# Kernel optimization log

Hardware: AMD Instinct MI355X
Metric: run time of the kernel (lower is better)

## Reference

```python
import jax, jax.numpy as jnp
import numpy as np

STATE_DIM = 64   # state_dim (N), N/2 complex modes
KLEN = 128       # L, learned impulse-response length
CH = 1           # channel_dim
BATCH = 32
T = 1048576      # sequence length (T > L -> FFT branch)
DT_MIN, DT_MAX = 0.001, 0.1


def setup_inputs() -> dict:
    key = jax.random.key(0)
    ks = jax.random.split(key, 7)
    N2 = STATE_DIM // 2
    x = jax.random.normal(ks[0], (BATCH, CH, T), dtype=jnp.float32)
    # HiPPO initialization: w = -0.5 + i * (1/pi) * N * (N/(1+2k) - 1)
    k = np.arange(N2)
    w_real = np.broadcast_to(np.float32(-0.5), (CH, N2)).copy()
    w_imag = np.broadcast_to(
        ((1.0 / np.pi) * STATE_DIM * (STATE_DIM / (1.0 + 2.0 * k) - 1.0)).astype(np.float32),
        (CH, N2)).copy()
    log_dt = (jax.random.uniform(ks[1], (CH, 1), dtype=jnp.float32)
              * (np.log(DT_MAX) - np.log(DT_MIN)) + np.log(DT_MIN))
    C_real = jax.random.normal(ks[2], (CH, 1, N2), dtype=jnp.float32) * 0.1
    C_imag = jax.random.normal(ks[3], (CH, 1, N2), dtype=jnp.float32) * 0.1
    B_real = jax.random.normal(ks[4], (CH, N2), dtype=jnp.float32)
    B_imag = jax.random.normal(ks[5], (CH, N2), dtype=jnp.float32)
    nrm = jnp.sqrt(jnp.sum(B_real ** 2 + B_imag ** 2, axis=-1, keepdims=True))
    B_real, B_imag = B_real / nrm, B_imag / nrm
    D = jax.random.normal(ks[6], (CH,), dtype=jnp.float32) * 0.1
    return {"azimuth_data": x,
            "w_real": jnp.asarray(w_real), "w_imag": jnp.asarray(w_imag),
            "log_dt": log_dt,
            "C_real": C_real, "C_imag": C_imag,
            "B_real": B_real, "B_imag": B_imag,
            "D": D}


def _ssm_kernel(w_real, w_imag, log_dt, C_real, C_imag, B_real, B_imag, D, L):
    """Vectorized equivalent of the per-step power recurrence: h_k = Re(sum_n C_n B_n A_n^k)."""
    w = w_real + 1j * w_imag                      # (CH, N2) complex eigenvalues
    dt = jnp.exp(log_dt)                          # (CH, 1)
    Cc = C_real + 1j * C_imag                     # (CH, 1, N2)
    Bc = B_real + 1j * B_imag                     # (CH, N2)
    dtA = dt[..., None] * w                       # (CH,1,1)*(CH,N2) -> (CH,1,N2)
    # coefficients C.squeeze(1) * B, with the same broadcast as torch: (CH,N2)*(CH,1,N2)->(CH,1,N2)
    coef = jnp.squeeze(Cc, axis=1) * (jnp.ones_like(dtA) * Bc)   # (CH,1,N2)
    ks = jnp.arange(L, dtype=dtA.real.dtype)                      # (L,)
    Ak = jnp.exp(dtA[..., None] * ks)                             # (CH,1,N2,L) = A_discrete**k
    h = jnp.real(jnp.sum(coef[..., None] * Ak, axis=-2))          # (CH,1,L)
    h = h.at[..., 0].add(D)                                       # hk[0] += D (broadcast (CH,1)+(CH,))
    return h[:, None]                                             # unsqueeze(1) -> (CH,1,1,L)


def reference(azimuth_data, w_real, w_imag, log_dt, C_real, C_imag, B_real, B_imag, D):
    Bsz, Cn, Tn = azimuth_data.shape
    kernel = _ssm_kernel(w_real, w_imag, log_dt, C_real, C_imag, B_real, B_imag, D, KLEN)
    pad = KLEN - 1
    x_padded = jnp.pad(azimuth_data, ((0, 0), (0, 0), (pad, 0)))   # causal left-pad
    L_conv = x_padded.shape[-1]
    x_f = jnp.fft.rfft(x_padded, n=L_conv)                         # (B, CH, F)
    k_f = jnp.fft.rfft(kernel, n=L_conv)                           # (CH, 1, 1, F)
    y_f = x_f * k_f                                                # broadcast -> (CH, B, 1, F)
    focused = jnp.fft.irfft(y_f, n=L_conv)[..., :Tn]               # (CH, B, 1, T) — matches torch broadcast
    return focused
```

## Files before the change

kernel.cpp:

```cpp
#include <hip/hip_runtime.h>

#define T_LEN  1048576
#define NROWS  32
#define NTAPS  128
#define N2     32
#define BLOCK  256
#define SEG    4096
#define SEGS_PER_ROW 256
#define HALO   256
#define NCH    11
#define STG_F32 (SEG + HALO)
#define STG_Q4  (STG_F32 / 4)
#define XH_BYTES 8704
#define SMEM_BYTES (XH_BYTES + 4 * 1024 * 4)

typedef __attribute__((ext_vector_type(8)))  _Float16 half8;
typedef __attribute__((ext_vector_type(2)))  __fp16   fp16x2;
typedef __attribute__((ext_vector_type(16))) float    f32x16;
typedef __attribute__((ext_vector_type(4)))  float    f32x4;

__device__ __forceinline__ int swz16(int q) { return q ^ ((q >> 3) & 7); }

__global__ __launch_bounds__(NTAPS) void ssm_taps(
    const float* __restrict__ w_real, const float* __restrict__ w_imag,
    const float* __restrict__ log_dt,
    const float* __restrict__ C_real, const float* __restrict__ C_imag,
    const float* __restrict__ B_real, const float* __restrict__ B_imag,
    const float* __restrict__ Dp, float* __restrict__ ws) {
  __shared__ float hsh[NTAPS];
  const int k = threadIdx.x;
  const float dt = expf(log_dt[0]);
  const float kf = (float)k;
  float acc = 0.f;
  for (int n = 0; n < N2; ++n) {
    const float a  = dt * w_real[n];
    const float b  = dt * w_imag[n];
    const float cr = C_real[n], ci = C_imag[n];
    const float br = B_real[n], bi = B_imag[n];
    const float coef_r = cr * br - ci * bi;
    const float coef_i = cr * bi + ci * br;
    const float e = expf(a * kf);
    float s, c;
    sincosf(b * kf, &s, &c);
    acc += e * (coef_r * c - coef_i * s);
  }
  if (k == 0) acc += Dp[0];
  ws[k]  = acc;
  hsh[k] = acc;
  __syncthreads();
  if (k < 64) {
    _Float16* AH = (_Float16*)(ws + NTAPS);
    const int m = k & 31, g = k >> 5;
    for (int c = 0; c < NCH; ++c)
      for (int i = 0; i < 8; ++i) {
        const int idx = m + 129 - 16 * c - 8 * g - i;
        const float v = (idx >= 0 && idx < NTAPS) ? hsh[idx] : 0.f;
        AH[(c * 64 + k) * 8 + i] = (_Float16)v;
      }
  }
}

__global__ __launch_bounds__(BLOCK, 6) void ssm_conv(
    const float* __restrict__ x, const float* __restrict__ ws,
    float* __restrict__ out) {
  __shared__ __align__(16) unsigned char smem[SMEM_BYTES];
  _Float16* xh    = (_Float16*)smem;
  float*    ebase = (float*)(smem + XH_BYTES);

  const int tid  = threadIdx.x;
  const int lane = tid & 63;
  const int wid  = tid >> 6;
  const int p    = lane & 31, g = lane >> 5;
  const int row  = blockIdx.x >> 8;
  const int jb   = blockIdx.x & 255;
  const int n0   = jb * SEG;
  const float* __restrict__ xrow = x + (size_t)row * T_LEN;

#pragma unroll
  for (int j = 0; j < 5; ++j) {
    const int q4 = tid + 256 * j;
    if (q4 < STG_Q4) {
      int gfi = n0 - HALO + 4 * q4;
      gfi = gfi < 0 ? 0 : gfi;
      const float4 f = *(const float4*)(xrow + gfi);
      const fp16x2 a = __builtin_amdgcn_cvt_pkrtz(f.x, f.y);
      const fp16x2 b = __builtin_amdgcn_cvt_pkrtz(f.z, f.w);
      uint2 w;
      w.x = __builtin_bit_cast(unsigned, a);
      w.y = __builtin_bit_cast(unsigned, b);
      const int c16 = q4 >> 1;
      *(uint2*)((char*)xh + swz16(c16) * 16 + (q4 & 1) * 8) = w;
    }
  }

  half8 A[NCH];
  const half8* __restrict__ wsA = (const half8*)(ws + NTAPS);
#pragma unroll
  for (int c = 0; c < NCH; ++c) A[c] = wsA[c * 64 + lane];

  __syncthreads();

  const int qb = wid * 128 + 4 * p + g;
  f32x16 acc = {};
#pragma unroll
  for (int c = 0; c < NCH; ++c) {
    const half8 B = *(const half8*)((char*)xh + swz16(qb + 2 * c) * 16);
    acc = __builtin_amdgcn_mfma_f32_32x32x16_f16(A[c], B, acc, 0, 0, 0);
  }

  float* ebuf = ebase + wid * 1024;
#pragma unroll
  for (int k = 0; k < 4; ++k) {
    const int q = p * 8 + 2 * k + g;
    float4 v;
    v.x = acc[4 * k];     v.y = acc[4 * k + 1];
    v.z = acc[4 * k + 2]; v.w = acc[4 * k + 3];
    *(float4*)(ebuf + (q ^ (p & 7)) * 4) = v;
  }
  float* __restrict__ obase = out + (size_t)row * T_LEN + n0 + wid * 1024;
#pragma unroll
  for (int pp = 0; pp < 4; ++pp) {
    const int o  = 4 * lane + 256 * pp;
    const int pc = o >> 5;
    const int q  = pc * 8 + (lane & 7);
    const f32x4 v = *(const f32x4*)(ebuf + (q ^ (pc & 7)) * 4);
    __builtin_nontemporal_store(v, (f32x4*)(obase + o));
  }

  if (jb == 0) {
    __syncthreads();
    const float* __restrict__ h = ws;
    if (tid < 254) {
      float a = 0.f;
      if (tid < 127) {
        for (int k = tid + 1; k < NTAPS; ++k)
          a += h[k] * xrow[T_LEN + tid - k];
      } else {
        for (int k = 0; k <= tid - 127; ++k)
          a += h[k] * xrow[tid - 127 - k];
      }
      out[(size_t)row * T_LEN + tid] = a;
    }
  }
}

extern "C" void kernel_launch(void* const* d_in, const int* in_sizes, int n_in,
                              void* d_out, int out_size, void* d_ws, size_t ws_size,
                              hipStream_t stream) {
  const float* x      = (const float*)d_in[0];
  const float* w_real = (const float*)d_in[1];
  const float* w_imag = (const float*)d_in[2];
  const float* log_dt = (const float*)d_in[3];
  const float* C_real = (const float*)d_in[4];
  const float* C_imag = (const float*)d_in[5];
  const float* B_real = (const float*)d_in[6];
  const float* B_imag = (const float*)d_in[7];
  const float* Dp     = (const float*)d_in[8];
  float* out = (float*)d_out;
  float* ws  = (float*)d_ws;

  ssm_taps<<<1, NTAPS, 0, stream>>>(w_real, w_imag, log_dt,
                                    C_real, C_imag, B_real, B_imag, Dp, ws);
  ssm_conv<<<NROWS * SEGS_PER_ROW, BLOCK, 0, stream>>>(x, ws, out);
}
```

Measured before the change: 66.11 us.

## Give each wave a private input window to drop the block barrier

Each wave now stages its own 1024-output window plus a 256-sample halo into a private LDS region, so the block-wide __syncthreads before the MFMA loop is no longer needed and waves can proceed independently. This costs redundant loading of overlapping halo data, about 14% more global reads and fp16 conversions, and a larger LDS footprint per block, which is why the occupancy hint drops from 6 to 4 blocks per SIMD. The tap-matrix loads are also moved ahead of the staging loop so they can overlap with it.

Result: no change. 67.16 us (+1.6%).

```diff
diff --git a/kernel.cpp b/kernel.cpp
--- a/kernel.cpp
+++ b/kernel.cpp
@@ -7,12 +7,13 @@
 #define BLOCK  256
 #define SEG    4096
 #define SEGS_PER_ROW 256
-#define HALO   256
 #define NCH    11
-#define STG_F32 (SEG + HALO)
-#define STG_Q4  (STG_F32 / 4)
-#define XH_BYTES 8704
-#define SMEM_BYTES (XH_BYTES + 4 * 1024 * 4)
+#define W_OUT  1024
+#define W_Q4   292
+#define XH_W_BYTES 2432
+#define EPI_W_BYTES 4096
+#define WAVE_BYTES (XH_W_BYTES + EPI_W_BYTES)
+#define SMEM_BYTES (4 * WAVE_BYTES)
 
 typedef __attribute__((ext_vector_type(8)))  _Float16 half8;
 typedef __attribute__((ext_vector_type(2)))  __fp16   fp16x2;
@@ -60,12 +61,10 @@
   }
 }
 
-__global__ __launch_bounds__(BLOCK, 6) void ssm_conv(
+__global__ __launch_bounds__(BLOCK, 4) void ssm_conv(
     const float* __restrict__ x, const float* __restrict__ ws,
     float* __restrict__ out) {
   __shared__ __align__(16) unsigned char smem[SMEM_BYTES];
-  _Float16* xh    = (_Float16*)smem;
-  float*    ebase = (float*)(smem + XH_BYTES);
 
   const int tid  = threadIdx.x;
   const int lane = tid & 63;
@@ -73,14 +72,22 @@
   const int p    = lane & 31, g = lane >> 5;
   const int row  = blockIdx.x >> 8;
   const int jb   = blockIdx.x & 255;
-  const int n0   = jb * SEG;
+  const int W0   = jb * SEG + wid * W_OUT;
   const float* __restrict__ xrow = x + (size_t)row * T_LEN;
+
+  char*  xw   = (char*)smem + wid * WAVE_BYTES;
+  float* ebuf = (float*)(xw + XH_W_BYTES);
+
+  half8 A[NCH];
+  const half8* __restrict__ wsA = (const half8*)(ws + NTAPS);
+#pragma unroll
+  for (int c = 0; c < NCH; ++c) A[c] = wsA[c * 64 + lane];
 
 #pragma unroll
   for (int j = 0; j < 5; ++j) {
-    const int q4 = tid + 256 * j;
-    if (q4 < STG_Q4) {
-      int gfi = n0 - HALO + 4 * q4;
+    const int q4 = lane + 64 * j;
+    if (q4 < W_Q4) {
+      int gfi = W0 - 256 + 4 * q4;
       gfi = gfi < 0 ? 0 : gfi;
       const float4 f = *(const float4*)(xrow + gfi);
       const fp16x2 a = __builtin_amdgcn_cvt_pkrtz(f.x, f.y);
@@ -88,27 +95,18 @@
       uint2 w;
       w.x = __builtin_bit_cast(unsigned, a);
       w.y = __builtin_bit_cast(unsigned, b);
-      const int c16 = q4 >> 1;
-      *(uint2*)((char*)xh + swz16(c16) * 16 + (q4 & 1) * 8) = w;
+      *(uint2*)(xw + swz16(q4 >> 1) * 16 + (q4 & 1) * 8) = w;
     }
   }
 
-  half8 A[NCH];
-  const half8* __restrict__ wsA = (const half8*)(ws + NTAPS);
-#pragma unroll
-  for (int c = 0; c < NCH; ++c) A[c] = wsA[c * 64 + lane];
-
-  __syncthreads();
-
-  const int qb = wid * 128 + 4 * p + g;
+  const int qb = 4 * p + g;
   f32x16 acc = {};
 #pragma unroll
   for (int c = 0; c < NCH; ++c) {
-    const half8 B = *(const half8*)((char*)xh + swz16(qb + 2 * c) * 16);
+    const half8 B = *(const half8*)(xw + swz16(qb + 2 * c) * 16);
     acc = __builtin_amdgcn_mfma_f32_32x32x16_f16(A[c], B, acc, 0, 0, 0);
   }
 
-  float* ebuf = ebase + wid * 1024;
 #pragma unroll
   for (int k = 0; k < 4; ++k) {
     const int q = p * 8 + 2 * k + g;
@@ -117,7 +115,7 @@
     v.z = acc[4 * k + 2]; v.w = acc[4 * k + 3];
     *(float4*)(ebuf + (q ^ (p & 7)) * 4) = v;
   }
-  float* __restrict__ obase = out + (size_t)row * T_LEN + n0 + wid * 1024;
+  float* __restrict__ obase = out + (size_t)row * T_LEN + W0;
 #pragma unroll
   for (int pp = 0; pp < 4; ++pp) {
     const int o  = 4 * lane + 256 * pp;
```
